# Kernel optimization log

Measured on AMD Instinct MI355X. Metric: run time of the kernel, lower is better.

The kernel has to match this reference:

```python
import jax, jax.numpy as jnp
import numpy as np

N_VARS = 512      # code length n (input_output_layer_size)
DV = 4            # variable-node degree
E = N_VARS * DV   # neurons = number of Tanner-graph edges = 2048
B = 8192          # batch of codewords
CLIP_TANH = 10.0
KL_SCALE = 5.0


def _build_masks():
    # edge e belongs to variable node var_idx[e]
    var_idx = np.repeat(np.arange(N_VARS), DV)          # [E]
    same_var = var_idx[:, None] == var_idx[None, :]     # [E,E]
    # v2c (odd->even) mask: edges sharing a variable node, excluding self-edge
    odd2even_mask = (same_var & ~np.eye(E, dtype=bool)).astype(np.float32)
    # skip-connection mask: LLR of variable v feeds every edge incident to v
    skip_mask = (np.arange(N_VARS)[:, None] == var_idx[None, :]).astype(np.float32)  # [n,E]
    return jnp.asarray(odd2even_mask), jnp.asarray(skip_mask)


def setup_inputs() -> dict:
    key = jax.random.key(0)
    k = jax.random.split(key, 6)
    w_odd2even_mask, w_skipconn2even_mask = _build_masks()
    return {
        "x": jax.random.normal(k[0], (B, E), dtype=jnp.float32),
        "llr": jax.random.normal(k[1], (B, N_VARS), dtype=jnp.float32),
        "odd_weights": jax.random.normal(k[2], (E, E), dtype=jnp.float32),
        "llr_weights": jax.random.normal(k[3], (N_VARS, E), dtype=jnp.float32),
        "dropout_logit": jax.random.uniform(k[4], (E,), dtype=jnp.float32),  # torch.rand init
        "u": jax.random.uniform(k[5], (E, E), dtype=jnp.float32),            # ARM uniform noise
        "w_odd2even_mask": w_odd2even_mask,
        "w_skipconn2even_mask": w_skipconn2even_mask,
    }


def reference(x, llr, odd_weights, llr_weights, dropout_logit, u,
              w_odd2even_mask, w_skipconn2even_mask):
    p = jax.nn.sigmoid(dropout_logit)                       # [E], broadcasts over rows of u
    total_mask = w_odd2even_mask * odd_weights              # [E,E]
    # ARM dropout: z ~ (u < sigmoid(logit)), z_tilde ~ (u > sigmoid(-logit))
    z = (u < p).astype(x.dtype)
    z_tilde = (u > jax.nn.sigmoid(-dropout_logit)).astype(x.dtype)
    msgs = x @ (total_mask * z)                             # [B,E]
    msgs_tilde = x @ (total_mask * z_tilde)                 # [B,E]
    llr_term = llr @ (w_skipconn2even_mask * llr_weights)   # [B,E]
    output = jnp.tanh(0.5 * jnp.clip(msgs + llr_term, -CLIP_TANH, CLIP_TANH))
    init_arm_tilde = jnp.tanh(0.5 * jnp.clip(msgs_tilde + llr_term, -CLIP_TANH, CLIP_TANH))
    # KL / entropy regularizer
    scaling1 = (KL_SCALE ** 2 / 2.0) * p                    # [E]
    first_layer_kl = scaling1 * jnp.sum(odd_weights ** 2, axis=1)  # ||W||_2 per row, squared
    H1 = -p * jnp.log(p) - (1.0 - p) * jnp.log(1.0 - p)
    kl_term = jnp.mean(first_layer_kl - H1)
    return output, init_arm_tilde, kl_term
```

## Files before the change

kernel.cpp:

```cpp
#include <hip/hip_runtime.h>
#include <math.h>

#define N_VARS 512
#define DV 4
#define EDGES 2048
#define BATCH 8192
#define CLIP_TANH 10.0f
#define ROWS 16

typedef float f32x4 __attribute__((ext_vector_type(4)));

__global__ __launch_bounds__(256) void prep_kernel(
    const float* __restrict__ odd_weights,
    const float* __restrict__ llr_weights,
    const float* __restrict__ dropout_logit,
    const float* __restrict__ u,
    const float* __restrict__ mask_oe,
    const float* __restrict__ mask_skip,
    f32x4* __restrict__ WZ,
    f32x4* __restrict__ WZT,
    float* __restrict__ LW,
    float* __restrict__ rowv)
{
    int blk = blockIdx.x;
    int t = threadIdx.x;

    if (blk < EDGES) {
        int e = blk;
        const f32x4* row = (const f32x4*)(odd_weights + (size_t)e * EDGES);
        float s = 0.0f;
#pragma unroll
        for (int i = t; i < EDGES / 4; i += 256) {
            f32x4 w = row[i];
            s = fmaf(w.x, w.x, s);
            s = fmaf(w.y, w.y, s);
            s = fmaf(w.z, w.z, s);
            s = fmaf(w.w, w.w, s);
        }
#pragma unroll
        for (int off = 32; off > 0; off >>= 1)
            s += __shfl_down(s, off, 64);
        __shared__ float red[4];
        if ((t & 63) == 0) red[t >> 6] = s;
        __syncthreads();
        if (t == 0) {
            float ss = red[0] + red[1] + red[2] + red[3];
            float logit = dropout_logit[e];
            float p = 1.0f / (1.0f + expf(-logit));
            float H1 = -p * logf(p) - (1.0f - p) * logf(1.0f - p);
            rowv[e] = 12.5f * p * ss - H1;
        }
    } else {
        int e = (blk - EDGES) * 256 + t;
        int v = e >> 2;
        int base = v << 2;

        float logit = dropout_logit[e];
        float p = 1.0f / (1.0f + expf(-logit));
        float q = 1.0f / (1.0f + expf(logit));

        f32x4 wz, wzt;
#pragma unroll
        for (int j = 0; j < 4; ++j) {
            size_t off = (size_t)(base + j) * EDGES + e;
            float w = odd_weights[off] * mask_oe[off];
            float uu = u[off];
            wz[j]  = (uu < p) ? w : 0.0f;
            wzt[j] = (uu > q) ? w : 0.0f;
        }
        WZ[e]  = wz;
        WZT[e] = wzt;

        size_t soff = (size_t)v * EDGES + e;
        LW[e] = llr_weights[soff] * mask_skip[soff];
    }
}

__device__ __forceinline__ float tanh_half(float m) {
    float t = __expf(m);
    return (t - 1.0f) * __builtin_amdgcn_rcpf(t + 1.0f);
}

__global__ __launch_bounds__(256) void main_kernel(
    const float* __restrict__ x,
    const float* __restrict__ llr,
    const f32x4* __restrict__ WZ,
    const f32x4* __restrict__ WZT,
    const float* __restrict__ LW,
    const float* __restrict__ rowv,
    float* __restrict__ out0,
    float* __restrict__ out1,
    float* __restrict__ kl)
{
    int idx = blockIdx.x * 256 + threadIdx.x;
    int v = idx & (N_VARS - 1);
    int b0 = (idx >> 9) * ROWS;

    f32x4 wz[4], wzt[4];
    float lw[4];
#pragma unroll
    for (int c = 0; c < 4; ++c) {
        int e = (v << 2) + c;
        wz[c]  = WZ[e];
        wzt[c] = WZT[e];
        lw[c]  = LW[e];
    }

    f32x4 x4[ROWS];
    float l[ROWS];
#pragma unroll
    for (int r = 0; r < ROWS; ++r) {
        x4[r] = ((const f32x4*)(x + (size_t)(b0 + r) * EDGES))[v];
        l[r]  = llr[(size_t)(b0 + r) * N_VARS + v];
    }

#pragma unroll
    for (int r = 0; r < ROWS; ++r) {
        f32x4 o0, o1;
#pragma unroll
        for (int c = 0; c < 4; ++c) {
            float lt = l[r] * lw[c];
            float m  = fmaf(x4[r].x, wz[c].x,  fmaf(x4[r].y, wz[c].y,
                       fmaf(x4[r].z, wz[c].z,  fmaf(x4[r].w, wz[c].w,  lt))));
            float mt = fmaf(x4[r].x, wzt[c].x, fmaf(x4[r].y, wzt[c].y,
                       fmaf(x4[r].z, wzt[c].z, fmaf(x4[r].w, wzt[c].w, lt))));
            m  = fminf(fmaxf(m,  -CLIP_TANH), CLIP_TANH);
            mt = fminf(fmaxf(mt, -CLIP_TANH), CLIP_TANH);
            o0[c] = tanh_half(m);
            o1[c] = tanh_half(mt);
        }
        __builtin_nontemporal_store(o0,
            &((f32x4*)(out0 + (size_t)(b0 + r) * EDGES))[v]);
        __builtin_nontemporal_store(o1,
            &((f32x4*)(out1 + (size_t)(b0 + r) * EDGES))[v]);
    }

    if (blockIdx.x == 0) {
        int t = threadIdx.x;
        float s = 0.0f;
#pragma unroll
        for (int i = t; i < EDGES; i += 256) s += rowv[i];
#pragma unroll
        for (int off = 32; off > 0; off >>= 1)
            s += __shfl_down(s, off, 64);
        __shared__ float red[4];
        if ((t & 63) == 0) red[t >> 6] = s;
        __syncthreads();
        if (t == 0) kl[0] = (red[0] + red[1] + red[2] + red[3]) / (float)EDGES;
    }
}

extern "C" void kernel_launch(void* const* d_in, const int* in_sizes, int n_in,
                              void* d_out, int out_size, void* d_ws, size_t ws_size,
                              hipStream_t stream) {
    const float* x             = (const float*)d_in[0];
    const float* llr           = (const float*)d_in[1];
    const float* odd_weights   = (const float*)d_in[2];
    const float* llr_weights   = (const float*)d_in[3];
    const float* dropout_logit = (const float*)d_in[4];
    const float* u             = (const float*)d_in[5];
    const float* mask_oe       = (const float*)d_in[6];
    const float* mask_skip     = (const float*)d_in[7];

    float* out0 = (float*)d_out;
    float* out1 = out0 + (size_t)BATCH * EDGES;
    float* kl   = out0 + (size_t)2 * BATCH * EDGES;

    char* ws = (char*)d_ws;
    f32x4* WZ  = (f32x4*)(ws);
    f32x4* WZT = (f32x4*)(ws + 32768);
    float* LW  = (float*)(ws + 65536);
    float* ROWV= (float*)(ws + 73728);

    prep_kernel<<<EDGES + EDGES / 256, 256, 0, stream>>>(
        odd_weights, llr_weights, dropout_logit, u, mask_oe, mask_skip,
        WZ, WZT, LW, ROWV);

    int threads = (BATCH / ROWS) * N_VARS;
    main_kernel<<<threads / 256, 256, 0, stream>>>(
        x, llr, WZ, WZT, LW, ROWV, out0, out1, kl);
}
```

Before: 44.10 us.

## Move KL row-norm reduction into main kernel with last-block final reduce

The per-row squared-norm and entropy computation over odd_weights moves out of the prep kernel into the main kernel, which has 1024 blocks, so each block handles two rows before its batch work. The final mean is done by whichever block finishes last, found with an atomic counter and a threadfence, instead of by block 0. This shrinks the prep kernel to 8 blocks and hides the 16MB weight-norm read behind the main streaming pass. In exchange every main block adds extra reads, barriers and an atomic, and the result depends on a counter that params_kernel resets on each launch.

```diff
diff --git a/kernel.cpp b/kernel.cpp
--- a/kernel.cpp
+++ b/kernel.cpp
@@ -7,10 +7,11 @@
 #define BATCH 8192
 #define CLIP_TANH 10.0f
 #define ROWS 16
+#define NBLK (BATCH / ROWS * N_VARS / 256)
 
 typedef float f32x4 __attribute__((ext_vector_type(4)));
 
-__global__ __launch_bounds__(256) void prep_kernel(
+__global__ __launch_bounds__(256) void params_kernel(
     const float* __restrict__ odd_weights,
     const float* __restrict__ llr_weights,
     const float* __restrict__ dropout_logit,
@@ -20,13 +21,60 @@
     f32x4* __restrict__ WZ,
     f32x4* __restrict__ WZT,
     float* __restrict__ LW,
-    float* __restrict__ rowv)
+    int*   __restrict__ counter)
 {
-    int blk = blockIdx.x;
+    int e = blockIdx.x * 256 + threadIdx.x;
+    if (e == 0) *counter = 0;
+
+    int v = e >> 2;
+    int base = v << 2;
+
+    float logit = dropout_logit[e];
+    float p = 1.0f / (1.0f + expf(-logit));
+    float q = 1.0f / (1.0f + expf(logit));
+
+    f32x4 wz, wzt;
+#pragma unroll
+    for (int j = 0; j < 4; ++j) {
+        size_t off = (size_t)(base + j) * EDGES + e;
+        float w = odd_weights[off] * mask_oe[off];
+        float uu = u[off];
+        wz[j]  = (uu < p) ? w : 0.0f;
+        wzt[j] = (uu > q) ? w : 0.0f;
+    }
+    WZ[e]  = wz;
+    WZT[e] = wzt;
+
+    size_t soff = (size_t)v * EDGES + e;
+    LW[e] = llr_weights[soff] * mask_skip[soff];
+}
+
+__device__ __forceinline__ float tanh_half(float m) {
+    float t = __expf(m);
+    return (t - 1.0f) * __builtin_amdgcn_rcpf(t + 1.0f);
+}
+
+__global__ __launch_bounds__(256) void main_kernel(
+    const float* __restrict__ x,
+    const float* __restrict__ llr,
+    const float* __restrict__ odd_weights,
+    const float* __restrict__ dropout_logit,
+    const f32x4* __restrict__ WZ,
+    const f32x4* __restrict__ WZT,
+    const float* __restrict__ LW,
+    float* __restrict__ rowv,
+    int*   __restrict__ counter,
+    float* __restrict__ out0,
+    float* __restrict__ out1,
+    float* __restrict__ kl)
+{
     int t = threadIdx.x;
+    __shared__ float red[4];
+    __shared__ int isLast;
 
-    if (blk < EDGES) {
-        int e = blk;
+#pragma unroll
+    for (int rr = 0; rr < 2; ++rr) {
+        int e = blockIdx.x * 2 + rr;
         const f32x4* row = (const f32x4*)(odd_weights + (size_t)e * EDGES);
         float s = 0.0f;
 #pragma unroll
@@ -40,7 +88,6 @@
 #pragma unroll
         for (int off = 32; off > 0; off >>= 1)
             s += __shfl_down(s, off, 64);
-        __shared__ float red[4];
         if ((t & 63) == 0) red[t >> 6] = s;
         __syncthreads();
         if (t == 0) {
@@ -50,49 +97,15 @@
             float H1 = -p * logf(p) - (1.0f - p) * logf(1.0f - p);
             rowv[e] = 12.5f * p * ss - H1;
         }
-    } else {
-        int e = (blk - EDGES) * 256 + t;
-        int v = e >> 2;
-        int base = v << 2;
+        __syncthreads();
+    }
+    if (t == 0) {
+        __threadfence();
+        int old = atomicAdd(counter, 1);
+        isLast = (old == NBLK - 1);
+    }
 
-        float logit = dropout_logit[e];
-        float p = 1.0f / (1.0f + expf(-logit));
-        float q = 1.0f / (1.0f + expf(logit));
-
-        f32x4 wz, wzt;
-#pragma unroll
-        for (int j = 0; j < 4; ++j) {
-            size_t off = (size_t)(base + j) * EDGES + e;
-            float w = odd_weights[off] * mask_oe[off];
-            float uu = u[off];
-            wz[j]  = (uu < p) ? w : 0.0f;
-            wzt[j] = (uu > q) ? w : 0.0f;
-        }
-        WZ[e]  = wz;
-        WZT[e] = wzt;
-
-        size_t soff = (size_t)v * EDGES + e;
-        LW[e] = llr_weights[soff] * mask_skip[soff];
-    }
-}
-
-__device__ __forceinline__ float tanh_half(float m) {
-    float t = __expf(m);
-    return (t - 1.0f) * __builtin_amdgcn_rcpf(t + 1.0f);
-}
-
-__global__ __launch_bounds__(256) void main_kernel(
-    const float* __restrict__ x,
-    const float* __restrict__ llr,
-    const f32x4* __restrict__ WZ,
-    const f32x4* __restrict__ WZT,
-    const float* __restrict__ LW,
-    const float* __restrict__ rowv,
-    float* __restrict__ out0,
-    float* __restrict__ out1,
-    float* __restrict__ kl)
-{
-    int idx = blockIdx.x * 256 + threadIdx.x;
+    int idx = blockIdx.x * 256 + t;
     int v = idx & (N_VARS - 1);
     int b0 = (idx >> 9) * ROWS;
 
@@ -135,15 +148,14 @@
             &((f32x4*)(out1 + (size_t)(b0 + r) * EDGES))[v]);
     }
 
-    if (blockIdx.x == 0) {
-        int t = threadIdx.x;
+    __syncthreads();
+    if (isLast) {
         float s = 0.0f;
-#pragma unroll
-        for (int i = t; i < EDGES; i += 256) s += rowv[i];
+        for (int i = t; i < EDGES; i += 256)
+            s += atomicAdd(&rowv[i], 0.0f);
 #pragma unroll
         for (int off = 32; off > 0; off >>= 1)
             s += __shfl_down(s, off, 64);
-        __shared__ float red[4];
         if ((t & 63) == 0) red[t >> 6] = s;
         __syncthreads();
         if (t == 0) kl[0] = (red[0] + red[1] + red[2] + red[3]) / (float)EDGES;
@@ -167,16 +179,17 @@
     float* kl   = out0 + (size_t)2 * BATCH * EDGES;
 
     char* ws = (char*)d_ws;
-    f32x4* WZ  = (f32x4*)(ws);
-    f32x4* WZT = (f32x4*)(ws + 32768);
-    float* LW  = (float*)(ws + 65536);
-    float* ROWV= (float*)(ws + 73728);
+    f32x4* WZ   = (f32x4*)(ws);
+    f32x4* WZT  = (f32x4*)(ws + 32768);
+    float* LW   = (float*)(ws + 65536);
+    float* ROWV = (float*)(ws + 73728);
+    int*   CNT  = (int*)  (ws + 81920);
 
-    prep_kernel<<<EDGES + EDGES / 256, 256, 0, stream>>>(
+    params_kernel<<<EDGES / 256, 256, 0, stream>>>(
         odd_weights, llr_weights, dropout_logit, u, mask_oe, mask_skip,
-        WZ, WZT, LW, ROWV);
+        WZ, WZT, LW, CNT);
 
-    int threads = (BATCH / ROWS) * N_VARS;
-    main_kernel<<<threads / 256, 256, 0, stream>>>(
-        x, llr, WZ, WZT, LW, ROWV, out0, out1, kl);
+    main_kernel<<<NBLK, 256, 0, stream>>>(
+        x, llr, odd_weights, dropout_logit, WZ, WZT, LW, ROWV, CNT,
+        out0, out1, kl);
 }
```

Measured after the change: 73.18 us. 1.66x slower.
